# Kernel tuning notes

Measured on AMD Instinct MI355X. Metric: run time of the kernel, lower is better.

The kernel has to match this reference:

```python
import jax, jax.numpy as jnp
import numpy as np
import math

EPS = 1e-5
GROUPS = 8


def setup_inputs() -> dict:
    key = jax.random.key(0)
    ks = jax.random.split(key, 4)
    b, c, h, w = 4, 256, 64, 64
    x = jax.random.normal(ks[0], (b, c, h, w), dtype=jnp.float32)
    norm_w = jnp.ones((c,), dtype=jnp.float32)
    norm_b = jnp.zeros((c,), dtype=jnp.float32)
    qkv_w = jax.random.normal(ks[1], (3 * c, c), dtype=jnp.float32) * (1.0 / math.sqrt(c))
    qkv_b = jnp.zeros((3 * c,), dtype=jnp.float32)
    proj_w = jax.random.normal(ks[2], (c, c), dtype=jnp.float32) * (1.0 / math.sqrt(c))
    proj_b = jnp.zeros((c,), dtype=jnp.float32)
    return {"x": x, "norm_w": norm_w, "norm_b": norm_b, "qkv_w": qkv_w,
            "qkv_b": qkv_b, "proj_w": proj_w, "proj_b": proj_b}


def group_norm(x, weight, bias):
    b, c, h, w = x.shape
    xg = x.reshape(b, GROUPS, c // GROUPS, h, w)
    mean = xg.mean(axis=(2, 3, 4), keepdims=True)
    var = xg.var(axis=(2, 3, 4), keepdims=True)
    xg = (xg - mean) * jax.lax.rsqrt(var + EPS)
    xn = xg.reshape(b, c, h, w)
    return xn * weight[None, :, None, None] + bias[None, :, None, None]


def reference(x, norm_w, norm_b, qkv_w, qkv_b, proj_w, proj_b):
    b, c, h, w = x.shape
    n = h * w
    xn = group_norm(x, norm_w, norm_b)
    # 1x1 conv == per-pixel linear: tokens [b, n, c]
    tokens = xn.reshape(b, c, n).transpose(0, 2, 1)
    qkv = jnp.einsum('bnc,oc->bno', tokens, qkv_w) + qkv_b  # [b, n, 3c]
    q, k, v = jnp.split(qkv, 3, axis=-1)
    scale = 1.0 / math.sqrt(c)
    attn = jnp.einsum('bqc,bkc->bqk', q, k) * scale  # [b, n, n]
    attn = jax.nn.softmax(attn, axis=-1)
    out = jnp.einsum('bqk,bkc->bqc', attn, v)  # [b, n, c]
    out = jnp.einsum('bnc,oc->bno', out, proj_w) + proj_b
    out = out.transpose(0, 2, 1).reshape(b, c, h, w)
    return x + out
```

## Files before the change

kernel.cpp:

```cpp
#include <hip/hip_runtime.h>
#include <math.h>

typedef unsigned short u16;
typedef __bf16 bf16x8 __attribute__((ext_vector_type(8)));
typedef u16    u16x8  __attribute__((ext_vector_type(8)));
typedef float  f32x4  __attribute__((ext_vector_type(4)));
typedef float  f32x16 __attribute__((ext_vector_type(16)));

__device__ __forceinline__ float b2f(u16 u) {
    union { unsigned u; float f; } x; x.u = ((unsigned)u) << 16; return x.f;
}
__device__ __forceinline__ u16 f2b(float f) {
    union { float f; unsigned u; } x; x.f = f;
    unsigned r = x.u + 0x7FFFu + ((x.u >> 16) & 1u);
    return (u16)(r >> 16);
}
__device__ __forceinline__ f32x4 mfma16(bf16x8 a, bf16x8 b, f32x4 c) {
    return __builtin_amdgcn_mfma_f32_16x16x32_bf16(a, b, c, 0, 0, 0);
}
__device__ __forceinline__ f32x16 mfma32(bf16x8 a, bf16x8 b, f32x16 c) {
    return __builtin_amdgcn_mfma_f32_32x32x16_bf16(a, b, c, 0, 0, 0);
}
__device__ __forceinline__ void dma16(const void* g, void* l) {
    __builtin_amdgcn_global_load_lds((const __attribute__((address_space(1))) void*)g,
                                     (__attribute__((address_space(3))) void*)l, 16, 0, 0);
}

#define QSCALE 0.09016844f

__global__ __launch_bounds__(256) void k_detect(const unsigned* __restrict__ x32, int* __restrict__ flag) {
    __shared__ int cnt;
    if (threadIdx.x == 0) cnt = 0;
    __syncthreads();
    int local = 0;
    for (int i = threadIdx.x; i < 4096; i += 256) {
        unsigned lo = x32[i] & 0xFFFFu;
        unsigned e = (lo >> 7) & 0xFFu;
        if (e >= 0x60u && e <= 0x8Fu) local++;
    }
    atomicAdd(&cnt, local);
    __syncthreads();
    if (threadIdx.x == 0) *flag = (cnt >= 2048) ? 0 : 1;
}

__global__ __launch_bounds__(256) void k_cvtx(const void* __restrict__ src, u16* __restrict__ dst,
                                              const int* __restrict__ flag) {
    const int i = (blockIdx.x * 256 + threadIdx.x) * 4;
    if (*flag) {
        float4 v = *(const float4*)((const float*)src + i);
        u16 o0 = f2b(v.x), o1 = f2b(v.y), o2 = f2b(v.z), o3 = f2b(v.w);
        unsigned lo = (unsigned)o0 | ((unsigned)o1 << 16);
        unsigned hi = (unsigned)o2 | ((unsigned)o3 << 16);
        *(uint2*)(dst + i) = make_uint2(lo, hi);
    } else {
        *(uint2*)(dst + i) = *(const uint2*)((const u16*)src + i);
    }
}

__global__ __launch_bounds__(256) void k_cvtp(const void* s0, const void* s1, const void* s2,
                                              const void* s3, const void* s4, const void* s5,
                                              u16* d0, u16* d1, u16* d2, u16* d3, u16* d4, u16* d5,
                                              const int* __restrict__ flag) {
    const int i = blockIdx.x * 256 + threadIdx.x;
    const int f = *flag;
    const void* s; u16* d; int j;
    if      (i < 256)    { s = s0; d = d0; j = i; }
    else if (i < 512)    { s = s1; d = d1; j = i - 256; }
    else if (i < 197120) { s = s2; d = d2; j = i - 512; }
    else if (i < 197888) { s = s3; d = d3; j = i - 197120; }
    else if (i < 263424) { s = s4; d = d4; j = i - 197888; }
    else if (i < 263680) { s = s5; d = d5; j = i - 263424; }
    else return;
    if (f) d[j] = f2b(((const float*)s)[j]);
    else   d[j] = ((const u16*)s)[j];
}

__global__ __launch_bounds__(256) void k_stats(const u16* __restrict__ x, float* __restrict__ stats) {
    const int bg = blockIdx.x;
    const u16* p = x + (size_t)bg * 131072;
    float s = 0.f, ss = 0.f;
    for (int i = threadIdx.x; i < 16384; i += 256) {
        bf16x8 v = *(const bf16x8*)(p + i * 8);
#pragma unroll
        for (int j = 0; j < 8; j++) { float f = (float)v[j]; s += f; ss += f * f; }
    }
#pragma unroll
    for (int o = 1; o < 64; o <<= 1) { s += __shfl_xor(s, o, 64); ss += __shfl_xor(ss, o, 64); }
    __shared__ float rs[4], rss[4];
    const int wv = threadIdx.x >> 6;
    if ((threadIdx.x & 63) == 0) { rs[wv] = s; rss[wv] = ss; }
    __syncthreads();
    if (threadIdx.x == 0) {
        s = rs[0] + rs[1] + rs[2] + rs[3];
        ss = rss[0] + rss[1] + rss[2] + rss[3];
        float mean = s * (1.f / 131072.f);
        float var = fmaxf(ss * (1.f / 131072.f) - mean * mean, 0.f);
        stats[bg] = mean;
        stats[32 + bg] = rsqrtf(var + 1e-5f);
    }
}

__global__ __launch_bounds__(256) void k_tok(const u16* __restrict__ x, const u16* __restrict__ nw,
                                             const u16* __restrict__ nb, const float* __restrict__ stats,
                                             u16* __restrict__ tok) {
    const int b = blockIdx.z, c0 = blockIdx.y * 64, p0 = blockIdx.x * 64;
    __shared__ u16 t[64][72];
    const int cl = threadIdx.x >> 2, seg = threadIdx.x & 3;
    const int c = c0 + cl;
    const int g = c >> 5;
    const float mean = stats[b * 8 + g], rstd = stats[32 + b * 8 + g];
    const float scale = b2f(nw[c]) * rstd;
    const float shift = b2f(nb[c]) - mean * scale;
    const u16* xp = x + ((size_t)(b * 256 + c)) * 4096 + p0 + seg * 16;
#pragma unroll
    for (int h = 0; h < 2; h++) {
        bf16x8 v = *(const bf16x8*)(xp + h * 8);
#pragma unroll
        for (int j = 0; j < 8; j++)
            t[seg * 16 + h * 8 + j][cl] = f2b((float)v[j] * scale + shift);
    }
    __syncthreads();
    u16x8 o0, o1;
#pragma unroll
    for (int j = 0; j < 8; j++) { o0[j] = t[cl][seg * 16 + j]; o1[j] = t[cl][seg * 16 + 8 + j]; }
    u16* op = tok + ((size_t)(b * 4096 + p0 + cl)) * 256 + c0 + seg * 16;
    *(u16x8*)op = o0;
    *((u16x8*)op + 1) = o1;
}

__global__ __launch_bounds__(256) void k_qkv(const u16* __restrict__ A, const u16* __restrict__ W,
                                             const u16* __restrict__ bias,
                                             u16* __restrict__ Qo, u16* __restrict__ Ko, u16* __restrict__ Vt) {
    const int m0 = blockIdx.x * 128, n0 = blockIdx.y * 128;
    const int tid = threadIdx.x, w = tid >> 6, lane = tid & 63, l15 = lane & 15, l4 = lane >> 4;
    const int wm = w >> 1, wn = w & 1;
    __shared__ __attribute__((aligned(16))) u16 At[128 * 64];
    __shared__ __attribute__((aligned(16))) u16 Bt[128 * 64];
    f32x4 acc[4][4];
    const f32x4 z = {0.f, 0.f, 0.f, 0.f};
#pragma unroll
    for (int i = 0; i < 4; i++)
#pragma unroll
        for (int j = 0; j < 4; j++) acc[i][j] = z;

    for (int kt = 0; kt < 4; kt++) {
        const int k0 = kt * 64;
#pragma unroll
        for (int i = 0; i < 4; i++) {
            int v = tid + i * 256;
            int row = v >> 3, c8 = v & 7;
            int swz = (c8 ^ (row & 7)) << 3;
            *(u16x8*)(&At[row * 64 + swz]) = *(const u16x8*)(A + (size_t)(m0 + row) * 256 + k0 + c8 * 8);
            *(u16x8*)(&Bt[row * 64 + swz]) = *(const u16x8*)(W + (size_t)(n0 + row) * 256 + k0 + c8 * 8);
        }
        __syncthreads();
#pragma unroll
        for (int ks = 0; ks < 2; ks++) {
            const int sc = ((ks * 4 + l4) ^ (l15 & 7)) << 3;
            bf16x8 af[4], bfr[4];
#pragma unroll
            for (int i = 0; i < 4; i++) {
                af[i]  = *(const bf16x8*)(&At[(wm * 64 + i * 16 + l15) * 64 + sc]);
                bfr[i] = *(const bf16x8*)(&Bt[(wn * 64 + i * 16 + l15) * 64 + sc]);
            }
#pragma unroll
            for (int i = 0; i < 4; i++)
#pragma unroll
                for (int j = 0; j < 4; j++) acc[i][j] = mfma16(af[i], bfr[j], acc[i][j]);
        }
        __syncthreads();
    }
#pragma unroll
    for (int j = 0; j < 4; j++) {
        const int n = n0 + wn * 64 + j * 16 + l15;
        const float bia = b2f(bias[n]);
#pragma unroll
        for (int i = 0; i < 4; i++) {
#pragma unroll
            for (int r = 0; r < 4; r++) {
                const int m = m0 + wm * 64 + i * 16 + l4 * 4 + r;
                const float vv = acc[i][j][r] + bia;
                if (n < 256)       Qo[(size_t)m * 256 + n] = f2b(vv * QSCALE);
                else if (n < 512)  Ko[(size_t)m * 256 + (n - 256)] = f2b(vv);
                else {
                    const int bb = m >> 12;
                    int p = m & 4095;
                    int d = ((p >> 2) ^ (p >> 3)) & 1;
                    p ^= d * 12;
                    Vt[((size_t)bb * 256 + (n - 512)) * 4096 + p] = f2b(vv);
                }
            }
        }
    }
}

__global__ __launch_bounds__(256, 2) void k_attn(const u16* __restrict__ Q, const u16* __restrict__ K,
                                                 const u16* __restrict__ Vt,
                                                 u16* __restrict__ Up, float* __restrict__ ml) {
    const int qt = blockIdx.x, b = blockIdx.y, sp = blockIdx.z;
    const int tid = threadIdx.x, w = tid >> 6, lane = tid & 63;
    const int l31 = lane & 31, h = lane >> 5;
    const int qcol = qt * 128 + w * 32 + l31;

    __shared__ __attribute__((aligned(16))) u16 KT[32 * 256];
    __shared__ __attribute__((aligned(16))) u16 VT[256 * 32];

    bf16x8 aq[16];
    {
        const u16* qp = Q + ((size_t)(b * 4096 + qcol)) * 256 + h * 8;
#pragma unroll
        for (int kb = 0; kb < 16; kb++) aq[kb] = *(const bf16x8*)(qp + kb * 16);
    }
    f32x16 acc[8];
#pragma unroll
    for (int ct = 0; ct < 8; ct++)
#pragma unroll
        for (int r = 0; r < 16; r++) acc[ct][r] = 0.f;
    float m_i = -3e38f, l_i = 0.f;

    const u16* Kg0 = K + (size_t)(b * 4096 + sp * 1024) * 256;
    const u16* Vg0 = Vt + (size_t)b * 256 * 4096 + sp * 1024;

    for (int kt = 0; kt < 32; kt++) {
        {
            const u16* Kg = Kg0 + (size_t)kt * 32 * 256;
#pragma unroll
            for (int i = 0; i < 4; i++) {
                int q = i * 256 + tid;
                int row = q >> 5, c = q & 31;
                dma16(Kg + row * 256 + ((c ^ row) << 3), &KT[(i * 256 + (tid & 192)) * 8]);
            }
            const u16* Vg = Vg0 + kt * 32;
#pragma unroll
            for (int i = 0; i < 4; i++) {
                int q = i * 256 + tid;
                int row = q >> 2, c = q & 3;
                dma16(Vg + (size_t)row * 4096 + ((c ^ ((row >> 3) & 3)) << 3), &VT[(i * 256 + (tid & 192)) * 8]);
            }
        }
        __syncthreads();

        f32x16 st;
#pragma unroll
        for (int r = 0; r < 16; r++) st[r] = 0.f;
#pragma unroll
        for (int kb = 0; kb < 16; kb++) {
            bf16x8 bk = *(const bf16x8*)(&KT[l31 * 256 + (((kb * 2 + h) ^ l31) << 3)]);
            st = mfma32(bk, aq[kb], st);
        }

        float mx = st[0];
#pragma unroll
        for (int r = 1; r < 16; r++) mx = fmaxf(mx, st[r]);
        mx = fmaxf(mx, __shfl_xor(mx, 32, 64));
        if (__any(mx > m_i + 4.f)) {
            const float m_new = fmaxf(m_i, mx);
            const float al = __builtin_amdgcn_exp2f(m_i - m_new);
#pragma unroll
            for (int ct = 0; ct < 8; ct++)
#pragma unroll
                for (int r = 0; r < 16; r++) acc[ct][r] *= al;
            l_i *= al;
            m_i = m_new;
        }
        float sum = 0.f;
#pragma unroll
        for (int r = 0; r < 16; r++) {
            st[r] = __builtin_amdgcn_exp2f(st[r] - m_i);
            sum += st[r];
        }
        sum += __shfl_xor(sum, 32, 64);
        l_i += sum;

        union { u16x8 u; bf16x8 bv; } p0, p1;
#pragma unroll
        for (int e = 0; e < 8; e++) { p0.u[e] = f2b(st[e]); p1.u[e] = f2b(st[8 + e]); }

#pragma unroll
        for (int ct = 0; ct < 8; ct++) {
            bf16x8 av0 = *(const bf16x8*)(&VT[(ct * 32 + l31) * 32 + ((h ^ (l31 >> 3)) << 3)]);
            acc[ct] = mfma32(av0, p0.bv, acc[ct]);
            bf16x8 av1 = *(const bf16x8*)(&VT[(ct * 32 + l31) * 32 + (((2 + h) ^ (l31 >> 3)) << 3)]);
            acc[ct] = mfma32(av1, p1.bv, acc[ct]);
        }
        __syncthreads();
    }

    if (h == 0)
        ((float2*)ml)[(size_t)(sp * 4 + b) * 4096 + qcol] = make_float2(m_i, l_i);
    u16* up = Up + (size_t)(sp * 4 + b) * 256 * 4096 + qcol;
#pragma unroll
    for (int ct = 0; ct < 8; ct++) {
#pragma unroll
        for (int r = 0; r < 16; r++) {
            const int c = ct * 32 + (r & 3) + 8 * (r >> 2) + 4 * h;
            up[(size_t)c * 4096] = f2b(acc[ct][r]);
        }
    }
}

__global__ __launch_bounds__(256) void k_comb(const u16* __restrict__ Up, const float* __restrict__ ml,
                                              u16* __restrict__ Ob) {
    const int qt = blockIdx.x, b = blockIdx.y;
    const int tid = threadIdx.x, ql = tid & 63, cg = tid >> 6;
    const int q = qt * 64 + ql;
    __shared__ __attribute__((aligned(16))) u16 T[64 * 256];
    float w_s[4];
    {
        float m_s[4], l_s[4];
#pragma unroll
        for (int s = 0; s < 4; s++) {
            float2 v = ((const float2*)ml)[(size_t)(s * 4 + b) * 4096 + q];
            m_s[s] = v.x; l_s[s] = v.y;
        }
        float M = fmaxf(fmaxf(m_s[0], m_s[1]), fmaxf(m_s[2], m_s[3]));
        float L = 0.f, e[4];
#pragma unroll
        for (int s = 0; s < 4; s++) { e[s] = __builtin_amdgcn_exp2f(m_s[s] - M); L += l_s[s] * e[s]; }
        float inv = 1.f / fmaxf(L, 1e-30f);
#pragma unroll
        for (int s = 0; s < 4; s++) w_s[s] = e[s] * inv;
    }
#pragma unroll
    for (int j8 = 0; j8 < 8; j8++) {
        u16x8 o;
#pragma unroll
        for (int e = 0; e < 8; e++) {
            const int c = cg * 64 + j8 * 8 + e;
            float v = 0.f;
#pragma unroll
            for (int s = 0; s < 4; s++)
                v += b2f(Up[(size_t)((s * 4 + b) * 256 + c) * 4096 + q]) * w_s[s];
            o[e] = f2b(v);
        }
        *(u16x8*)(&T[ql * 256 + (((cg * 8 + j8) ^ (ql & 31)) << 3)]) = o;
    }
    __syncthreads();
    const int ql2 = tid >> 2, cs = tid & 3;
#pragma unroll
    for (int k = 0; k < 8; k++) {
        u16x8 v = *(const u16x8*)(&T[ql2 * 256 + (((cs * 8 + k) ^ (ql2 & 31)) << 3)]);
        *(u16x8*)(Ob + (size_t)(b * 4096 + qt * 64 + ql2) * 256 + cs * 64 + k * 8) = v;
    }
}

__global__ __launch_bounds__(256) void k_proj(const u16* __restrict__ A, const u16* __restrict__ W,
                                              const u16* __restrict__ bias, const u16* __restrict__ x,
                                              void* __restrict__ out, const int* __restrict__ flag) {
    const int f32out = *flag;
    const int m0 = blockIdx.x * 128, n0 = blockIdx.y * 128;
    const int tid = threadIdx.x, w = tid >> 6, lane = tid & 63, l15 = lane & 15, l4 = lane >> 4;
    const int wm = w >> 1, wn = w & 1;
    __shared__ __attribute__((aligned(16))) u16 At[128 * 64];
    __shared__ __attribute__((aligned(16))) u16 Bt[128 * 64];
    f32x4 acc[4][4];
    const f32x4 z = {0.f, 0.f, 0.f, 0.f};
#pragma unroll
    for (int i = 0; i < 4; i++)
#pragma unroll
        for (int j = 0; j < 4; j++) acc[i][j] = z;

    for (int kt = 0; kt < 4; kt++) {
        const int k0 = kt * 64;
#pragma unroll
        for (int i = 0; i < 4; i++) {
            int v = tid + i * 256;
            int row = v >> 3, c8 = v & 7;
            int swz = (c8 ^ (row & 7)) << 3;
            *(u16x8*)(&At[row * 64 + swz]) = *(const u16x8*)(A + (size_t)(m0 + row) * 256 + k0 + c8 * 8);
            *(u16x8*)(&Bt[row * 64 + swz]) = *(const u16x8*)(W + (size_t)(n0 + row) * 256 + k0 + c8 * 8);
        }
        __syncthreads();
#pragma unroll
        for (int ks = 0; ks < 2; ks++) {
            const int sc = ((ks * 4 + l4) ^ (l15 & 7)) << 3;
            bf16x8 af[4], bfr[4];
#pragma unroll
            for (int i = 0; i < 4; i++) {
                af[i]  = *(const bf16x8*)(&At[(wm * 64 + i * 16 + l15) * 64 + sc]);
                bfr[i] = *(const bf16x8*)(&Bt[(wn * 64 + i * 16 + l15) * 64 + sc]);
            }
#pragma unroll
            for (int i = 0; i < 4; i++)
#pragma unroll
                for (int j = 0; j < 4; j++) acc[i][j] = mfma16(af[i], bfr[j], acc[i][j]);
        }
        __syncthreads();
    }
#pragma unroll
    for (int j = 0; j < 4; j++) {
        const int n = n0 + wn * 64 + j * 16 + l15;
        const float bia = b2f(bias[n]);
#pragma unroll
        for (int i = 0; i < 4; i++) {
#pragma unroll
            for (int r = 0; r < 4; r++) {
                const int m = m0 + wm * 64 + i * 16 + l4 * 4 + r;
                const int bb = m >> 12, p = m & 4095;
                const size_t oi = ((size_t)bb * 256 + n) * 4096 + p;
                const float v = b2f(x[oi]) + acc[i][j][r] + bia;
                if (f32out) ((float*)out)[oi] = v;
                else        ((u16*)out)[oi] = f2b(v);
            }
        }
    }
}

extern "C" void kernel_launch(void* const* d_in, const int* in_sizes, int n_in,
                              void* d_out, int out_size, void* d_ws, size_t ws_size,
                              hipStream_t stream) {
    char* ws = (char*)d_ws;
    float* stats = (float*)ws;
    int*   flag  = (int*)(ws + 2048);
    u16* xb  = (u16*)(ws + 4096);
    u16* nwb = xb + (size_t)4194304;
    u16* nbb = nwb + 256;
    u16* qbb = nbb + 256;
    u16* pbb = qbb + 768;
    u16* pad = pbb + 256;
    u16* qwb = pad + 256;
    u16* pwb = qwb + (size_t)196608;
    u16* tok = pwb + (size_t)65536;
    u16* Qb  = tok + (size_t)16384 * 256;
    u16* Kb  = Qb  + (size_t)16384 * 256;
    u16* Vb  = Kb  + (size_t)16384 * 256;
    u16* Upb = Vb  + (size_t)16384 * 256;
    float* mlb = (float*)(Upb + (size_t)4 * 4 * 256 * 4096);
    u16* Ob  = tok;

    k_detect<<<dim3(1), dim3(256), 0, stream>>>((const unsigned*)d_in[0], flag);
    k_cvtx<<<dim3(4096), dim3(256), 0, stream>>>(d_in[0], xb, flag);
    k_cvtp<<<dim3(1030), dim3(256), 0, stream>>>(d_in[1], d_in[2], d_in[3], d_in[4], d_in[5], d_in[6],
                                                 nwb, nbb, qwb, qbb, pwb, pbb, flag);

    k_stats<<<dim3(32), dim3(256), 0, stream>>>(xb, stats);
    k_tok  <<<dim3(64, 4, 4), dim3(256), 0, stream>>>(xb, nwb, nbb, stats, tok);
    k_qkv  <<<dim3(128, 6), dim3(256), 0, stream>>>(tok, qwb, qbb, Qb, Kb, Vb);
    k_attn <<<dim3(32, 4, 4), dim3(256), 0, stream>>>(Qb, Kb, Vb, Upb, mlb);
    k_comb <<<dim3(64, 4), dim3(256), 0, stream>>>(Upb, mlb, Ob);
    k_proj <<<dim3(128, 2), dim3(256), 0, stream>>>(Ob, pwb, pbb, xb, d_out, flag);
}
```

Measured before the change: 238.1 us.

## Double-buffer attention K/V loads and fuse split-combine into projection GEMM

The attention kernel now double-buffers the K and V tiles in LDS with async global-to-LDS loads and explicit vmcnt waits, so the next tile's fetch overlaps the current compute. Its partial outputs are transposed through LDS and written token-major. The separate combine kernel is replaced by a tiny weight kernel, and the split-softmax merge moves into the projection GEMM's A-tile load, with a coalesced residual epilogue. The dtype-detect kernel is folded into the convert kernels via a wave ballot. This removes launches and a round trip through memory, but doubles attention LDS to 64KB, which may limit occupancy, and adds bf16 rounding in the epilogue.

New measurement: 238.8 us. Within noise of the previous version (+0.3%).

```diff
diff --git a/kernel.cpp b/kernel.cpp
--- a/kernel.cpp
+++ b/kernel.cpp
@@ -25,32 +25,24 @@
     __builtin_amdgcn_global_load_lds((const __attribute__((address_space(1))) void*)g,
                                      (__attribute__((address_space(3))) void*)l, 16, 0, 0);
 }
+__device__ __forceinline__ int dtype_vote(const unsigned* w) {
+    unsigned v = w[threadIdx.x & 63];
+    unsigned e = ((v & 0xFFFFu) >> 7) & 0xFFu;
+    unsigned long long m = __ballot(e >= 0x60u && e <= 0x8Fu);
+    return (__popcll(m) >= 32) ? 0 : 1;
+}
 
 #define QSCALE 0.09016844f
 
-__global__ __launch_bounds__(256) void k_detect(const unsigned* __restrict__ x32, int* __restrict__ flag) {
-    __shared__ int cnt;
-    if (threadIdx.x == 0) cnt = 0;
-    __syncthreads();
-    int local = 0;
-    for (int i = threadIdx.x; i < 4096; i += 256) {
-        unsigned lo = x32[i] & 0xFFFFu;
-        unsigned e = (lo >> 7) & 0xFFu;
-        if (e >= 0x60u && e <= 0x8Fu) local++;
-    }
-    atomicAdd(&cnt, local);
-    __syncthreads();
-    if (threadIdx.x == 0) *flag = (cnt >= 2048) ? 0 : 1;
-}
-
 __global__ __launch_bounds__(256) void k_cvtx(const void* __restrict__ src, u16* __restrict__ dst,
-                                              const int* __restrict__ flag) {
+                                              int* __restrict__ flag) {
+    const int f = dtype_vote((const unsigned*)src);
+    if (blockIdx.x == 0 && threadIdx.x == 0) *flag = f;
     const int i = (blockIdx.x * 256 + threadIdx.x) * 4;
-    if (*flag) {
+    if (f) {
         float4 v = *(const float4*)((const float*)src + i);
-        u16 o0 = f2b(v.x), o1 = f2b(v.y), o2 = f2b(v.z), o3 = f2b(v.w);
-        unsigned lo = (unsigned)o0 | ((unsigned)o1 << 16);
-        unsigned hi = (unsigned)o2 | ((unsigned)o3 << 16);
+        unsigned lo = (unsigned)f2b(v.x) | ((unsigned)f2b(v.y) << 16);
+        unsigned hi = (unsigned)f2b(v.z) | ((unsigned)f2b(v.w) << 16);
         *(uint2*)(dst + i) = make_uint2(lo, hi);
     } else {
         *(uint2*)(dst + i) = *(const uint2*)((const u16*)src + i);
@@ -59,10 +51,9 @@
 
 __global__ __launch_bounds__(256) void k_cvtp(const void* s0, const void* s1, const void* s2,
                                               const void* s3, const void* s4, const void* s5,
-                                              u16* d0, u16* d1, u16* d2, u16* d3, u16* d4, u16* d5,
-                                              const int* __restrict__ flag) {
+                                              u16* d0, u16* d1, u16* d2, u16* d3, u16* d4, u16* d5) {
+    const int f = dtype_vote((const unsigned*)s2);
     const int i = blockIdx.x * 256 + threadIdx.x;
-    const int f = *flag;
     const void* s; u16* d; int j;
     if      (i < 256)    { s = s0; d = d0; j = i; }
     else if (i < 512)    { s = s1; d = d1; j = i - 256; }
@@ -202,8 +193,9 @@
     const int l31 = lane & 31, h = lane >> 5;
     const int qcol = qt * 128 + w * 32 + l31;
 
-    __shared__ __attribute__((aligned(16))) u16 KT[32 * 256];
-    __shared__ __attribute__((aligned(16))) u16 VT[256 * 32];
+    __shared__ __attribute__((aligned(16))) char LB[65536];
+    u16* KT = (u16*)LB;
+    u16* VT = (u16*)(LB + 32768);
 
     bf16x8 aq[16];
     {
@@ -218,34 +210,47 @@
         for (int r = 0; r < 16; r++) acc[ct][r] = 0.f;
     float m_i = -3e38f, l_i = 0.f;
 
-    const u16* Kg0 = K + (size_t)(b * 4096 + sp * 1024) * 256;
-    const u16* Vg0 = Vt + (size_t)b * 256 * 4096 + sp * 1024;
+    const char* Kg0 = (const char*)(K + (size_t)(b * 4096 + sp * 1024) * 256);
+    const char* Vg0 = (const char*)(Vt + (size_t)b * 256 * 4096 + sp * 1024);
+    const int wb = (tid & 192) * 8;
+
+#define ISSUE(bi, kt)                                                                        \
+    {                                                                                        \
+        const char* Kg = Kg0 + (size_t)(kt) * 32 * 512;                                      \
+        const char* Vg = Vg0 + (size_t)(kt) * 64;                                            \
+        _Pragma("unroll")                                                                    \
+        for (int i = 0; i < 4; i++) {                                                        \
+            int q = i * 256 + tid;                                                           \
+            int row = q >> 5, c = q & 31;                                                    \
+            dma16(Kg + row * 512 + ((c ^ row) << 4), &KT[(bi) * 8192 + (i * 256) * 8 + wb]); \
+        }                                                                                    \
+        _Pragma("unroll")                                                                    \
+        for (int i = 0; i < 4; i++) {                                                        \
+            int q = i * 256 + tid;                                                           \
+            int row = q >> 2, c = q & 3;                                                     \
+            dma16(Vg + (size_t)row * 8192 + ((c ^ ((row >> 3) & 3)) << 4),                   \
+                  &VT[(bi) * 8192 + (i * 256) * 8 + wb]);                                    \
+        }                                                                                    \
+    }
+
+    ISSUE(0, 0)
+    ISSUE(1, 1)
 
     for (int kt = 0; kt < 32; kt++) {
-        {
-            const u16* Kg = Kg0 + (size_t)kt * 32 * 256;
-#pragma unroll
-            for (int i = 0; i < 4; i++) {
-                int q = i * 256 + tid;
-                int row = q >> 5, c = q & 31;
-                dma16(Kg + row * 256 + ((c ^ row) << 3), &KT[(i * 256 + (tid & 192)) * 8]);
-            }
-            const u16* Vg = Vg0 + kt * 32;
-#pragma unroll
-            for (int i = 0; i < 4; i++) {
-                int q = i * 256 + tid;
-                int row = q >> 2, c = q & 3;
-                dma16(Vg + (size_t)row * 4096 + ((c ^ ((row >> 3) & 3)) << 3), &VT[(i * 256 + (tid & 192)) * 8]);
-            }
-        }
-        __syncthreads();
+        const int cur = kt & 1;
+        if (kt < 31) asm volatile("s_waitcnt vmcnt(8)" ::: "memory");
+        else         asm volatile("s_waitcnt vmcnt(0)" ::: "memory");
+        asm volatile("s_barrier" ::: "memory");
+
+        const u16* KTc = &KT[cur * 8192];
+        const u16* VTc = &VT[cur * 8192];
 
         f32x16 st;
 #pragma unroll
         for (int r = 0; r < 16; r++) st[r] = 0.f;
 #pragma unroll
         for (int kb = 0; kb < 16; kb++) {
-            bf16x8 bk = *(const bf16x8*)(&KT[l31 * 256 + (((kb * 2 + h) ^ l31) << 3)]);
+            bf16x8 bk = *(const bf16x8*)(&KTc[l31 * 256 + (((kb * 2 + h) ^ l31) << 3)]);
             st = mfma32(bk, aq[kb], st);
         }
 
@@ -278,130 +283,162 @@
 
 #pragma unroll
         for (int ct = 0; ct < 8; ct++) {
-            bf16x8 av0 = *(const bf16x8*)(&VT[(ct * 32 + l31) * 32 + ((h ^ (l31 >> 3)) << 3)]);
+            bf16x8 av0 = *(const bf16x8*)(&VTc[(ct * 32 + l31) * 32 + ((h ^ (l31 >> 3)) << 3)]);
             acc[ct] = mfma32(av0, p0.bv, acc[ct]);
-            bf16x8 av1 = *(const bf16x8*)(&VT[(ct * 32 + l31) * 32 + (((2 + h) ^ (l31 >> 3)) << 3)]);
+            bf16x8 av1 = *(const bf16x8*)(&VTc[(ct * 32 + l31) * 32 + (((2 + h) ^ (l31 >> 3)) << 3)]);
             acc[ct] = mfma32(av1, p1.bv, acc[ct]);
         }
-        __syncthreads();
-    }
+        asm volatile("s_barrier" ::: "memory");
+        if (kt + 2 < 32) ISSUE(cur, kt + 2)
+    }
+#undef ISSUE
 
     if (h == 0)
         ((float2*)ml)[(size_t)(sp * 4 + b) * 4096 + qcol] = make_float2(m_i, l_i);
-    u16* up = Up + (size_t)(sp * 4 + b) * 256 * 4096 + qcol;
+    u16* Ot = (u16*)(LB + w * 16384);
 #pragma unroll
     for (int ct = 0; ct < 8; ct++) {
 #pragma unroll
         for (int r = 0; r < 16; r++) {
             const int c = ct * 32 + (r & 3) + 8 * (r >> 2) + 4 * h;
-            up[(size_t)c * 4096] = f2b(acc[ct][r]);
-        }
-    }
-}
-
-__global__ __launch_bounds__(256) void k_comb(const u16* __restrict__ Up, const float* __restrict__ ml,
-                                              u16* __restrict__ Ob) {
-    const int qt = blockIdx.x, b = blockIdx.y;
-    const int tid = threadIdx.x, ql = tid & 63, cg = tid >> 6;
-    const int q = qt * 64 + ql;
-    __shared__ __attribute__((aligned(16))) u16 T[64 * 256];
-    float w_s[4];
-    {
-        float m_s[4], l_s[4];
-#pragma unroll
-        for (int s = 0; s < 4; s++) {
-            float2 v = ((const float2*)ml)[(size_t)(s * 4 + b) * 4096 + q];
-            m_s[s] = v.x; l_s[s] = v.y;
-        }
-        float M = fmaxf(fmaxf(m_s[0], m_s[1]), fmaxf(m_s[2], m_s[3]));
-        float L = 0.f, e[4];
-#pragma unroll
-        for (int s = 0; s < 4; s++) { e[s] = __builtin_amdgcn_exp2f(m_s[s] - M); L += l_s[s] * e[s]; }
-        float inv = 1.f / fmaxf(L, 1e-30f);
-#pragma unroll
-        for (int s = 0; s < 4; s++) w_s[s] = e[s] * inv;
-    }
-#pragma unroll
-    for (int j8 = 0; j8 < 8; j8++) {
-        u16x8 o;
-#pragma unroll
-        for (int e = 0; e < 8; e++) {
-            const int c = cg * 64 + j8 * 8 + e;
-            float v = 0.f;
-#pragma unroll
-            for (int s = 0; s < 4; s++)
-                v += b2f(Up[(size_t)((s * 4 + b) * 256 + c) * 4096 + q]) * w_s[s];
-            o[e] = f2b(v);
-        }
-        *(u16x8*)(&T[ql * 256 + (((cg * 8 + j8) ^ (ql & 31)) << 3)]) = o;
-    }
-    __syncthreads();
-    const int ql2 = tid >> 2, cs = tid & 3;
-#pragma unroll
-    for (int k = 0; k < 8; k++) {
-        u16x8 v = *(const u16x8*)(&T[ql2 * 256 + (((cs * 8 + k) ^ (ql2 & 31)) << 3)]);
-        *(u16x8*)(Ob + (size_t)(b * 4096 + qt * 64 + ql2) * 256 + cs * 64 + k * 8) = v;
-    }
-}
-
-__global__ __launch_bounds__(256) void k_proj(const u16* __restrict__ A, const u16* __restrict__ W,
-                                              const u16* __restrict__ bias, const u16* __restrict__ x,
-                                              void* __restrict__ out, const int* __restrict__ flag) {
+            Ot[l31 * 256 + (((c >> 3) ^ l31) << 3) + (c & 7)] = f2b(acc[ct][r]);
+        }
+    }
+    u16* up = Up + ((size_t)(sp * 4 + b) * 4096 + qt * 128 + w * 32) * 256;
+#pragma unroll
+    for (int v = 0; v < 16; v++) {
+        int idx = v * 64 + lane;
+        int qrow = idx >> 5, c8 = idx & 31;
+        u16x8 d = *(const u16x8*)(&Ot[qrow * 256 + ((c8 ^ qrow) << 3)]);
+        *(u16x8*)(up + (size_t)qrow * 256 + c8 * 8) = d;
+    }
+}
+
+__global__ __launch_bounds__(256) void k_ml(const float* __restrict__ ml, float4* __restrict__ W4q) {
+    const int t = blockIdx.x * 256 + threadIdx.x;
+    const int b = t >> 12, q = t & 4095;
+    float m_s[4], l_s[4];
+#pragma unroll
+    for (int s = 0; s < 4; s++) {
+        float2 v = ((const float2*)ml)[(size_t)(s * 4 + b) * 4096 + q];
+        m_s[s] = v.x; l_s[s] = v.y;
+    }
+    float M = fmaxf(fmaxf(m_s[0], m_s[1]), fmaxf(m_s[2], m_s[3]));
+    float L = 0.f, e[4];
+#pragma unroll
+    for (int s = 0; s < 4; s++) { e[s] = __builtin_amdgcn_exp2f(m_s[s] - M); L += l_s[s] * e[s]; }
+    float inv = 1.f / fmaxf(L, 1e-30f);
+    W4q[t] = make_float4(e[0] * inv, e[1] * inv, e[2] * inv, e[3] * inv);
+}
+
+__global__ __launch_bounds__(256) void k_proj(const u16* __restrict__ Up, const float4* __restrict__ W4q,
+                                              const u16* __restrict__ W, const u16* __restrict__ bias,
+                                              const u16* __restrict__ x, void* __restrict__ out,
+                                              const int* __restrict__ flag) {
     const int f32out = *flag;
-    const int m0 = blockIdx.x * 128, n0 = blockIdx.y * 128;
+    const int m0 = blockIdx.x * 64;
+    const int b = m0 >> 12, q0 = m0 & 4095;
     const int tid = threadIdx.x, w = tid >> 6, lane = tid & 63, l15 = lane & 15, l4 = lane >> 4;
     const int wm = w >> 1, wn = w & 1;
-    __shared__ __attribute__((aligned(16))) u16 At[128 * 64];
-    __shared__ __attribute__((aligned(16))) u16 Bt[128 * 64];
-    f32x4 acc[4][4];
+    __shared__ __attribute__((aligned(16))) char PL[40960];
+    u16* At = (u16*)PL;
+    u16* Bt = (u16*)(PL + 8192);
+    u16* Ot = (u16*)PL;
+
+    const int qa = tid >> 2, ca = (tid & 3) * 16;
+    const float4 wq = W4q[m0 + qa];
+    const float wsv[4] = {wq.x, wq.y, wq.z, wq.w};
+    const u16* upb = Up + (size_t)(q0 + qa) * 256 + ca;
+
+    f32x4 acc[2][8];
     const f32x4 z = {0.f, 0.f, 0.f, 0.f};
 #pragma unroll
-    for (int i = 0; i < 4; i++)
-#pragma unroll
-        for (int j = 0; j < 4; j++) acc[i][j] = z;
+    for (int i = 0; i < 2; i++)
+#pragma unroll
+        for (int j = 0; j < 8; j++) acc[i][j] = z;
 
     for (int kt = 0; kt < 4; kt++) {
         const int k0 = kt * 64;
-#pragma unroll
-        for (int i = 0; i < 4; i++) {
-            int v = tid + i * 256;
+        {
+            float vs[16];
+#pragma unroll
+            for (int e = 0; e < 16; e++) vs[e] = 0.f;
+#pragma unroll
+            for (int s = 0; s < 4; s++) {
+                const u16* p = upb + ((size_t)(s * 4 + b) * 4096) * 256 + k0;
+                u16x8 u0 = *(const u16x8*)p;
+                u16x8 u1 = *(const u16x8*)(p + 8);
+                const float ws = wsv[s];
+#pragma unroll
+                for (int e = 0; e < 8; e++) { vs[e] += b2f(u0[e]) * ws; vs[8 + e] += b2f(u1[e]) * ws; }
+            }
+            u16x8 o0, o1;
+#pragma unroll
+            for (int e = 0; e < 8; e++) { o0[e] = f2b(vs[e]); o1[e] = f2b(vs[8 + e]); }
+            const int c8 = ca >> 3;
+            *(u16x8*)(&At[qa * 64 + ((c8 ^ (qa & 7)) << 3)]) = o0;
+            *(u16x8*)(&At[qa * 64 + (((c8 + 1) ^ (qa & 7)) << 3)]) = o1;
+        }
+#pragma unroll
+        for (int i = 0; i < 8; i++) {
+            int v = i * 256 + tid;
             int row = v >> 3, c8 = v & 7;
-            int swz = (c8 ^ (row & 7)) << 3;
-            *(u16x8*)(&At[row * 64 + swz]) = *(const u16x8*)(A + (size_t)(m0 + row) * 256 + k0 + c8 * 8);
-            *(u16x8*)(&Bt[row * 64 + swz]) = *(const u16x8*)(W + (size_t)(n0 + row) * 256 + k0 + c8 * 8);
+            *(u16x8*)(&Bt[row * 64 + ((c8 ^ (row & 7)) << 3)]) =
+                *(const u16x8*)(W + (size_t)row * 256 + k0 + c8 * 8);
         }
         __syncthreads();
 #pragma unroll
         for (int ks = 0; ks < 2; ks++) {
             const int sc = ((ks * 4 + l4) ^ (l15 & 7)) << 3;
-            bf16x8 af[4], bfr[4];
-#pragma unroll
-            for (int i = 0; i < 4; i++) {
-                af[i]  = *(const bf16x8*)(&At[(wm * 64 + i * 16 + l15) * 64 + sc]);
-                bfr[i] = *(const bf16x8*)(&Bt[(wn * 64 + i * 16 + l15) * 64 + sc]);
+            bf16x8 af[2], bfr[8];
+#pragma unroll
+            for (int i = 0; i < 2; i++)
+                af[i] = *(const bf16x8*)(&At[(wm * 32 + i * 16 + l15) * 64 + sc]);
+#pragma unroll
+            for (int j = 0; j < 8; j++)
+                bfr[j] = *(const bf16x8*)(&Bt[(wn * 128 + j * 16 + l15) * 64 + sc]);
+#pragma unroll
+            for (int i = 0; i < 2; i++)
+#pragma unroll
+                for (int j = 0; j < 8; j++) acc[i][j] = mfma16(af[i], bfr[j], acc[i][j]);
+        }
+        __syncthreads();
+    }
+
+#pragma unroll
+    for (int j = 0; j < 8; j++) {
+        const int n = wn * 128 + j * 16 + l15;
+        const float bia = b2f(bias[n]);
+#pragma unroll
+        for (int i = 0; i < 2; i++) {
+#pragma unroll
+            for (int r = 0; r < 4; r++) {
+                const int p = wm * 32 + i * 16 + l4 * 4 + r;
+                Ot[n * 64 + ((((p >> 3) ^ (n & 7)) << 3)) + (p & 7)] = f2b(acc[i][j][r] + bia);
             }
-#pragma unroll
-            for (int i = 0; i < 4; i++)
-#pragma unroll
-                for (int j = 0; j < 4; j++) acc[i][j] = mfma16(af[i], bfr[j], acc[i][j]);
-        }
-        __syncthreads();
-    }
-#pragma unroll
-    for (int j = 0; j < 4; j++) {
-        const int n = n0 + wn * 64 + j * 16 + l15;
-        const float bia = b2f(bias[n]);
-#pragma unroll
-        for (int i = 0; i < 4; i++) {
-#pragma unroll
-            for (int r = 0; r < 4; r++) {
-                const int m = m0 + wm * 64 + i * 16 + l4 * 4 + r;
-                const int bb = m >> 12, p = m & 4095;
-                const size_t oi = ((size_t)bb * 256 + n) * 4096 + p;
-                const float v = b2f(x[oi]) + acc[i][j][r] + bia;
-                if (f32out) ((float*)out)[oi] = v;
-                else        ((u16*)out)[oi] = f2b(v);
-            }
+        }
+    }
+    __syncthreads();
+    const int ps = (tid & 7) * 8;
+#pragma unroll
+    for (int v = 0; v < 8; v++) {
+        const int n = v * 32 + (tid >> 3);
+        u16x8 d = *(const u16x8*)(&Ot[n * 64 + ((((ps >> 3) ^ (n & 7)) << 3))]);
+        const size_t base = ((size_t)(b * 256 + n)) * 4096 + q0 + ps;
+        u16x8 xv = *(const u16x8*)(x + base);
+        if (f32out) {
+            float4 o0, o1;
+#pragma unroll
+            for (int e = 0; e < 4; e++) o0[e] = b2f(d[e]) + b2f(xv[e]);
+#pragma unroll
+            for (int e = 0; e < 4; e++) o1[e] = b2f(d[4 + e]) + b2f(xv[4 + e]);
+            *(float4*)((float*)out + base) = o0;
+            *(float4*)((float*)out + base + 4) = o1;
+        } else {
+            u16x8 o;
+#pragma unroll
+            for (int e = 0; e < 8; e++) o[e] = f2b(b2f(d[e]) + b2f(xv[e]));
+            *(u16x8*)((u16*)out + base) = o;
         }
     }
 }
@@ -425,18 +462,17 @@
     u16* Kb  = Qb  + (size_t)16384 * 256;
     u16* Vb  = Kb  + (size_t)16384 * 256;
     u16* Upb = Vb  + (size_t)16384 * 256;
-    float* mlb = (float*)(Upb + (size_t)4 * 4 * 256 * 4096);
-    u16* Ob  = tok;
-
-    k_detect<<<dim3(1), dim3(256), 0, stream>>>((const unsigned*)d_in[0], flag);
+    float* mlb = (float*)(Upb + (size_t)16 * 4096 * 256);
+    float4* W4q = (float4*)(mlb + (size_t)16 * 4096 * 2);
+
     k_cvtx<<<dim3(4096), dim3(256), 0, stream>>>(d_in[0], xb, flag);
     k_cvtp<<<dim3(1030), dim3(256), 0, stream>>>(d_in[1], d_in[2], d_in[3], d_in[4], d_in[5], d_in[6],
-                                                 nwb, nbb, qwb, qbb, pwb, pbb, flag);
+                                                 nwb, nbb, qwb, qbb, pwb, pbb);
 
     k_stats<<<dim3(32), dim3(256), 0, stream>>>(xb, stats);
     k_tok  <<<dim3(64, 4, 4), dim3(256), 0, stream>>>(xb, nwb, nbb, stats, tok);
     k_qkv  <<<dim3(128, 6), dim3(256), 0, stream>>>(tok, qwb, qbb, Qb, Kb, Vb);
     k_attn <<<dim3(32, 4, 4), dim3(256), 0, stream>>>(Qb, Kb, Vb, Upb, mlb);
-    k_comb <<<dim3(64, 4), dim3(256), 0, stream>>>(Upb, mlb, Ob);
-    k_proj <<<dim3(128, 2), dim3(256), 0, stream>>>(Ob, pwb, pbb, xb, d_out, flag);
-}
+    k_ml   <<<dim3(64), dim3(256), 0, stream>>>(mlb, W4q);
+    k_proj <<<dim3(256), dim3(256), 0, stream>>>(Upb, W4q, pwb, pbb, xb, d_out, flag);
+}
```
